# Performance work log

Hardware: AMD Instinct MI355X
Metric: run time of the kernel (lower is better)

The kernel has to match this reference:

```python
import jax
jax.config.update("jax_enable_x64", True)
import jax.numpy as jnp
import numpy as np

SAMPLE_RATE = 44100
HOP = 512
B, N_MELS, T = 8, 128, 2048
L = T * HOP  # 1,048,576 samples


def _lerp_up(x, out_len):
    # torch F.interpolate(mode='linear', align_corners=True): [B,C,Tin]->[B,C,out_len]
    t_in = x.shape[-1]
    pos = jnp.arange(out_len, dtype=jnp.float64) * ((t_in - 1) / (out_len - 1))
    i0 = jnp.floor(pos).astype(jnp.int32)
    i1 = jnp.minimum(i0 + 1, t_in - 1)
    w = (pos - i0).astype(x.dtype)
    return x[..., i0] * (1 - w) + x[..., i1] * w


def _conv1d(x, w, b, pad):
    y = jax.lax.conv_general_dilated(x, w, (1,), [(pad, pad)],
                                     dimension_numbers=("NCH", "OIH", "NCH"))
    return y + b[None, :, None]


def setup_inputs() -> dict:
    key = jax.random.key(0)
    ks = jax.random.split(key, 9)
    mel_frames = jax.random.normal(ks[0], (B, N_MELS, T), dtype=jnp.float32)
    # realistic f0: 80..380 Hz
    f0_frames = 80.0 + 300.0 * jax.random.uniform(ks[1], (B, T), dtype=jnp.float32)
    noise = jax.random.normal(ks[2], (B, L), dtype=jnp.float32)
    w1 = jax.random.normal(ks[3], (128, N_MELS, 7), dtype=jnp.float32) * 0.05
    b1 = jnp.zeros((128,), jnp.float32)
    w2 = jax.random.normal(ks[4], (128, 128, 3), dtype=jnp.float32) * 0.05
    b2 = jnp.zeros((128,), jnp.float32)
    w3 = jax.random.normal(ks[5], (2, 128, 3), dtype=jnp.float32) * 0.05
    b3 = jnp.zeros((2,), jnp.float32)
    return {"mel_frames": mel_frames, "f0_frames": f0_frames, "noise": noise,
            "w1": w1, "b1": b1, "w2": w2, "b2": b2, "w3": w3, "b3": b3}


def reference(mel_frames, f0_frames, noise, w1, b1, w2, b2, w3, b3):
    # --- comb source ---
    f0 = _lerp_up(f0_frames[:, None, :], L)  # [B,1,L]
    phase = jnp.cumsum(f0.astype(jnp.float64) / SAMPLE_RATE, axis=-1)
    phase = phase - jnp.round(phase)
    phase = phase.astype(f0.dtype)
    combtooth = jnp.sinc(SAMPLE_RATE * phase / (f0 + 1e-8))[:, 0, :]  # [B,L]
    # --- magnitude network ---
    h = jax.nn.leaky_relu(_conv1d(mel_frames, w1, b1, 3), 0.2)
    h = jax.nn.leaky_relu(_conv1d(h, w2, b2, 1), 0.2)
    mags = jnp.clip(_conv1d(h, w3, b3, 1), 0.0, 1.0)  # [B,2,T]
    mags = _lerp_up(mags, L)  # [B,2,L]
    noise_sig = jnp.clip(noise * mags[:, 0, :], -1.0, 1.0)
    comb_sig = jnp.clip(combtooth * mags[:, 1, :], -1.0, 1.0)
    signal = jnp.clip(noise_sig + comb_sig, -1.0, 1.0)
    return (signal[:, None, :], (comb_sig[:, None, :], noise_sig[:, None, :]))
```

## Files before the change

### kernel.cpp

```cpp
#include <hip/hip_runtime.h>
#include <math.h>

#define BATCH 8
#define NMEL 128
#define TT 2048
#define LL 1048576
#define NCHUNK 256
#define CHUNK 4096

static constexpr double RATIO  = 2047.0 / 1048575.0;
static constexpr float  RATIOF = (float)(2047.0 / 1048575.0);
static constexpr double INV_SR = 1.0 / 44100.0;

__global__ __launch_bounds__(256) void wtrans_kernel(
    const float* __restrict__ w1, const float* __restrict__ w2,
    float* __restrict__ w1t, float* __restrict__ w2t)
{
    int i = blockIdx.x * 256 + threadIdx.x;
    if (i < 896 * 128) {
        int m = i >> 7, co = i & 127;
        w1t[i] = w1[co * 896 + m];
    }
    if (i < 384 * 128) {
        int m = i >> 7, co = i & 127;
        w2t[i] = w2[co * 384 + m];
    }
}

#define CONV_FMA(acc, wq, xv, K) \
    _Pragma("unroll") \
    for (int k = 0; k < K; ++k) { \
        float wv0 = wq[k].x, wv1 = wq[k].y, wv2 = wq[k].z, wv3 = wq[k].w; \
        _Pragma("unroll") \
        for (int i = 0; i < 5; ++i) { \
            acc[0][i] = fmaf(wv0, xv[i + k], acc[0][i]); \
            acc[1][i] = fmaf(wv1, xv[i + k], acc[1][i]); \
            acc[2][i] = fmaf(wv2, xv[i + k], acc[2][i]); \
            acc[3][i] = fmaf(wv3, xv[i + k], acc[3][i]); } }

#define XSTR 48
#define HSTR 44
__global__ __launch_bounds__(256, 3) void conv_chunk_kernel(
    const float* __restrict__ mel,
    const float* __restrict__ w1t,
    const float* __restrict__ b1,
    const float* __restrict__ w2t,
    const float* __restrict__ b2,
    const float* __restrict__ w3,
    const float* __restrict__ b3,
    float* __restrict__ mags,
    const float* __restrict__ f0f,
    double* __restrict__ sums)
{
    __shared__ __align__(16) float smem[NMEL * XSTR + NMEL * HSTR];
    int tid = threadIdx.x;
    int lane = tid & 63, wid = tid >> 6;

    if (blockIdx.x >= 512) {
        int cb = blockIdx.x - 512;
        int b = cb >> 8;
        int c = cb & (NCHUNK - 1);
        const float* row = f0f + b * TT;
        int start = c * CHUNK + tid * 16;
        double pos0 = (double)start * RATIO;
        int i0s = (int)pos0;
        float wb = (float)(pos0 - (double)i0s);
        int ib = i0s + 1 > TT - 1 ? TT - 1 : i0s + 1;
        int ic = i0s + 2 > TT - 1 ? TT - 1 : i0s + 2;
        float f0a = row[i0s], f0b = row[ib], f0c = row[ic];
        double s = 0.0;
        #pragma unroll
        for (int i = 0; i < 16; ++i) {
            float wi = wb + (float)i * RATIOF;
            bool hi = wi >= 1.0f;
            float w = hi ? wi - 1.0f : wi;
            float xa = hi ? f0b : f0a, xb = hi ? f0c : f0b;
            float f0 = xa * (1.0f - w) + xb * w;
            s += (double)f0 * INV_SR;
        }
        #pragma unroll
        for (int off = 32; off > 0; off >>= 1) s += __shfl_down(s, (unsigned)off, 64);
        double* dred = (double*)smem;
        if (lane == 0) dred[wid] = s;
        __syncthreads();
        if (tid == 0) sums[cb] = dred[0] + dred[1] + dred[2] + dred[3];
        return;
    }

    float* Xs  = smem;
    float* H1  = smem + NMEL * XSTR;
    float* H2  = smem;
    float* red = smem + NMEL * XSTR;

    int b  = blockIdx.x >> 6;
    int t0 = (blockIdx.x & 63) * 32;
    const float* melb = mel + (size_t)b * NMEL * TT;

    #pragma unroll
    for (int it = 0; it < 6; ++it) {
        int idx = tid + it * 256;
        int ci = idx / 12, q = idx - ci * 12;
        int t = t0 - 8 + q * 4;
        float4 v = make_float4(0.f, 0.f, 0.f, 0.f);
        if (t >= 0 && t + 3 < TT) v = *(const float4*)(melb + ci * TT + t);
        *(float4*)(&Xs[ci * XSTR + q * 4]) = v;
    }
    if (tid < 128) { H1[tid * HSTR + 0] = 0.f; H1[tid * HSTR + 41] = 0.f; }
    __syncthreads();

    int cog = tid >> 3;
    int tg  = tid & 7;
    int xbase = 1 + tg * 5;

    {
        float acc[4][5];
        #pragma unroll
        for (int j = 0; j < 4; ++j) {
            float bj = b1[cog * 4 + j];
            #pragma unroll
            for (int i = 0; i < 5; ++i) acc[j][i] = bj;
        }
        const float* wb_ = w1t + cog * 4;
        float xvA[11], xvB[11];
        float4 wA[7], wB[7];
        #pragma unroll
        for (int i = 0; i < 11; ++i) xvA[i] = Xs[xbase + i];
        #pragma unroll
        for (int k = 0; k < 7; ++k) wA[k] = *(const float4*)(wb_ + (size_t)k * 128);
        for (int ci = 0; ci < NMEL; ci += 2) {
            int c1 = ci + 1;
            #pragma unroll
            for (int i = 0; i < 11; ++i) xvB[i] = Xs[c1 * XSTR + xbase + i];
            #pragma unroll
            for (int k = 0; k < 7; ++k) wB[k] = *(const float4*)(wb_ + (size_t)(c1 * 7 + k) * 128);
            CONV_FMA(acc, wA, xvA, 7)
            int c2 = ci + 2 < NMEL ? ci + 2 : NMEL - 1;
            #pragma unroll
            for (int i = 0; i < 11; ++i) xvA[i] = Xs[c2 * XSTR + xbase + i];
            #pragma unroll
            for (int k = 0; k < 7; ++k) wA[k] = *(const float4*)(wb_ + (size_t)(c2 * 7 + k) * 128);
            CONV_FMA(acc, wB, xvB, 7)
        }
        #pragma unroll
        for (int j = 0; j < 4; ++j)
            #pragma unroll
            for (int i = 0; i < 5; ++i) {
                int t = t0 - 4 + tg * 5 + i;
                float v = acc[j][i];
                v = v > 0.0f ? v : 0.2f * v;
                if (t < 0 || t >= TT) v = 0.0f;
                H1[(cog * 4 + j) * HSTR + 1 + tg * 5 + i] = v;
            }
    }
    __syncthreads();

    {
        float acc[4][5];
        #pragma unroll
        for (int j = 0; j < 4; ++j) {
            float bj = b2[cog * 4 + j];
            #pragma unroll
            for (int i = 0; i < 5; ++i) acc[j][i] = bj;
        }
        int hbase = tg * 5;
        const float* wb_ = w2t + cog * 4;
        float xvA[7], xvB[7];
        float4 wA[3], wB[3];
        #pragma unroll
        for (int i = 0; i < 7; ++i) xvA[i] = H1[hbase + i];
        #pragma unroll
        for (int k = 0; k < 3; ++k) wA[k] = *(const float4*)(wb_ + (size_t)k * 128);
        for (int ci = 0; ci < NMEL; ci += 2) {
            int c1 = ci + 1;
            #pragma unroll
            for (int i = 0; i < 7; ++i) xvB[i] = H1[c1 * HSTR + hbase + i];
            #pragma unroll
            for (int k = 0; k < 3; ++k) wB[k] = *(const float4*)(wb_ + (size_t)(c1 * 3 + k) * 128);
            CONV_FMA(acc, wA, xvA, 3)
            int c2 = ci + 2 < NMEL ? ci + 2 : NMEL - 1;
            #pragma unroll
            for (int i = 0; i < 7; ++i) xvA[i] = H1[c2 * HSTR + hbase + i];
            #pragma unroll
            for (int k = 0; k < 3; ++k) wA[k] = *(const float4*)(wb_ + (size_t)(c2 * 3 + k) * 128);
            CONV_FMA(acc, wB, xvB, 3)
        }
        #pragma unroll
        for (int j = 0; j < 4; ++j)
            #pragma unroll
            for (int i = 0; i < 5; ++i) {
                int t = t0 - 4 + tg * 5 + i;
                float v = acc[j][i];
                v = v > 0.0f ? v : 0.2f * v;
                if (t < 0 || t >= TT) v = 0.0f;
                H2[(cog * 4 + j) * HSTR + tg * 5 + i] = v;
            }
    }
    __syncthreads();

    {
        int o   = tid >> 7;
        int cig = (tid >> 5) & 3;
        int tt  = tid & 31;
        float a = 0.0f;
        for (int cl = 0; cl < 32; ++cl) {
            int ci = cig * 32 + cl;
            #pragma unroll
            for (int k = 0; k < 3; ++k)
                a = fmaf(w3[o * 384 + ci * 3 + k], H2[ci * HSTR + tt + 3 + k], a);
        }
        red[(o * 4 + cig) * 32 + tt] = a;
    }
    __syncthreads();
    if (tid < 64) {
        int o = tid >> 5, tt = tid & 31;
        float s = b3[o] + red[(o * 4 + 0) * 32 + tt] + red[(o * 4 + 1) * 32 + tt]
                        + red[(o * 4 + 2) * 32 + tt] + red[(o * 4 + 3) * 32 + tt];
        s = fminf(fmaxf(s, 0.0f), 1.0f);
        mags[((size_t)b * 2 + o) * TT + t0 + tt] = s;
    }
}

__device__ __forceinline__ int swz4(int g) { return g ^ ((g >> 3) & 7); }

__global__ __launch_bounds__(256, 4) void final_kernel(
    const float* __restrict__ f0f,
    const float* __restrict__ noise,
    const float* __restrict__ mags,
    const double* __restrict__ sums,
    float* __restrict__ out)
{
    int b = blockIdx.x >> 8;
    int c = blockIdx.x & (NCHUNK - 1);
    const float* row = f0f + b * TT;
    int tid = threadIdx.x;
    int lane = tid & 63, wid = tid >> 6;
    __shared__ float4 fracsV[CHUNK / 4];
    __shared__ double wsumP[4], wsumA[4];

    int chunkBase = c * CHUNK;
    int start = chunkBase + tid * 16;

    double part = (tid < c) ? sums[b * NCHUNK + tid] : 0.0;
    #pragma unroll
    for (int off = 32; off > 0; off >>= 1) part += __shfl_down(part, (unsigned)off, 64);
    if (lane == 0) wsumP[wid] = part;

    double pos0 = (double)start * RATIO;
    int i0s = (int)pos0;
    float wb = (float)(pos0 - (double)i0s);
    int ibk = i0s + 1 > TT - 1 ? TT - 1 : i0s + 1;
    int ick = i0s + 2 > TT - 1 ? TT - 1 : i0s + 2;
    float f0a = row[i0s], f0b = row[ibk], f0c = row[ick];
    float f0v[16];
    double s = 0.0;
    #pragma unroll
    for (int i = 0; i < 16; ++i) {
        float wi = wb + (float)i * RATIOF;
        bool hi = wi >= 1.0f;
        float w = hi ? wi - 1.0f : wi;
        float xa = hi ? f0b : f0a, xb = hi ? f0c : f0b;
        f0v[i] = xa * (1.0f - w) + xb * w;
        s += (double)f0v[i] * INV_SR;
    }
    double incl = s;
    #pragma unroll
    for (int off = 1; off < 64; off <<= 1) {
        double v = __shfl_up(incl, (unsigned)off, 64);
        if (lane >= off) incl += v;
    }
    if (lane == 63) wsumA[wid] = incl;
    __syncthreads();
    double run = wsumP[0] + wsumP[1] + wsumP[2] + wsumP[3] + (incl - s);
    for (int w = 0; w < wid; ++w) run += wsumA[w];

    float fb[4];
    #pragma unroll
    for (int i = 0; i < 16; ++i) {
        run += (double)f0v[i] * INV_SR;
        double fr = run - rint(run);
        fb[i & 3] = (float)fr;
        if ((i & 3) == 3)
            fracsV[swz4(tid * 4 + (i >> 2))] = make_float4(fb[0], fb[1], fb[2], fb[3]);
    }
    __syncthreads();

    const size_t BL = (size_t)BATCH * LL;
    const size_t outBase = (size_t)b * LL;
    const float* m0row = mags + (size_t)b * 2 * TT;
    const float* m1row = m0row + TT;

    #pragma unroll
    for (int g = 0; g < 4; ++g) {
        int G = g * 256 + tid;
        int n0 = chunkBase + G * 4;
        float4 fr4 = fracsV[swz4(G)];
        const float* frp = (const float*)&fr4;
        float4 nz4 = *(const float4*)(noise + outBase + n0);
        const float* nzp = (const float*)&nz4;

        double posg = (double)n0 * RATIO;
        int i0a = (int)posg;
        float wf = (float)(posg - (double)i0a);
        int ib = i0a + 1 > TT - 1 ? TT - 1 : i0a + 1;
        int ic = i0a + 2 > TT - 1 ? TT - 1 : i0a + 2;
        float g0a = row[i0a],   g0b = row[ib],   g0c = row[ic];
        float m0a = m0row[i0a], m0b = m0row[ib], m0c = m0row[ic];
        float m1a = m1row[i0a], m1b = m1row[ib], m1c = m1row[ic];

        float so[4], co_[4], no_[4];
        #pragma unroll
        for (int j = 0; j < 4; ++j) {
            float wj = wf + (float)j * RATIOF;
            bool hi = wj >= 1.0f;
            float w = hi ? wj - 1.0f : wj;
            float xa = hi ? g0b : g0a, xb = hi ? g0c : g0b;
            float f0 = xa * (1.0f - w) + xb * w;
            float ya = hi ? m0b : m0a, yb = hi ? m0c : m0b;
            float m0 = ya * (1.0f - w) + yb * w;
            float za = hi ? m1b : m1a, zb = hi ? m1c : m1b;
            float m1 = za * (1.0f - w) + zb * w;

            float ph = frp[j];
            float x  = 44100.0f * ph * __builtin_amdgcn_rcpf(f0 + 1e-8f);
            float px = 3.14159265358979323f * x;
            float rr = 0.5f * x;
            float rf = rr - rintf(rr);
            float sn;
            asm("v_sin_f32 %0, %1" : "=v"(sn) : "v"(rf));
            float comb = (x == 0.0f) ? 1.0f : sn * __builtin_amdgcn_rcpf(px);

            float ns = fminf(fmaxf(nzp[j] * m0, -1.0f), 1.0f);
            float cs = fminf(fmaxf(comb * m1, -1.0f), 1.0f);
            so[j] = fminf(fmaxf(ns + cs, -1.0f), 1.0f);
            co_[j] = cs; no_[j] = ns;
        }
        *(float4*)(out + outBase + n0)          = make_float4(so[0], so[1], so[2], so[3]);
        *(float4*)(out + BL + outBase + n0)     = make_float4(co_[0], co_[1], co_[2], co_[3]);
        *(float4*)(out + 2 * BL + outBase + n0) = make_float4(no_[0], no_[1], no_[2], no_[3]);
    }
}

extern "C" void kernel_launch(void* const* d_in, const int* in_sizes, int n_in,
                              void* d_out, int out_size, void* d_ws, size_t ws_size,
                              hipStream_t stream) {
    const float* mel   = (const float*)d_in[0];
    const float* f0f   = (const float*)d_in[1];
    const float* noise = (const float*)d_in[2];
    const float* w1    = (const float*)d_in[3];
    const float* b1    = (const float*)d_in[4];
    const float* w2    = (const float*)d_in[5];
    const float* b2    = (const float*)d_in[6];
    const float* w3    = (const float*)d_in[7];
    const float* b3    = (const float*)d_in[8];
    float* out = (float*)d_out;

    float* w1t  = (float*)d_ws;
    float* w2t  = w1t + 896 * 128;
    float* mags = w2t + 384 * 128;
    double* sums = (double*)(mags + BATCH * 2 * TT);

    wtrans_kernel<<<(896 * 128 + 255) / 256, 256, 0, stream>>>(w1, w2, w1t, w2t);
    conv_chunk_kernel<<<512 + BATCH * NCHUNK, 256, 0, stream>>>(
        mel, w1t, b1, w2t, b2, w3, b3, mags, f0f, sums);
    final_kernel<<<BATCH * NCHUNK, 256, 0, stream>>>(f0f, noise, mags, sums, out);
}
```

Before: 261.6 us.

## Split final kernel into phase and output passes; simplify conv loops

The final kernel is split in two. One kernel computes the wrapped phase fractions and writes them to a global workspace buffer of B*L floats. A second kernel reads them back together with noise and mags to produce the outputs. This removes the shared-memory staging and a block barrier, at the cost of an extra 32 MB global write and read plus one more launch. The conv loops also drop manual double-buffering in favour of a simple loop with unroll 2, leaving scheduling to the compiler.

Result: no change. 265.8 us (+1.6%).

```diff
diff --git a/kernel.cpp b/kernel.cpp
--- a/kernel.cpp
+++ b/kernel.cpp
@@ -26,17 +26,6 @@
         w2t[i] = w2[co * 384 + m];
     }
 }
-
-#define CONV_FMA(acc, wq, xv, K) \
-    _Pragma("unroll") \
-    for (int k = 0; k < K; ++k) { \
-        float wv0 = wq[k].x, wv1 = wq[k].y, wv2 = wq[k].z, wv3 = wq[k].w; \
-        _Pragma("unroll") \
-        for (int i = 0; i < 5; ++i) { \
-            acc[0][i] = fmaf(wv0, xv[i + k], acc[0][i]); \
-            acc[1][i] = fmaf(wv1, xv[i + k], acc[1][i]); \
-            acc[2][i] = fmaf(wv2, xv[i + k], acc[2][i]); \
-            acc[3][i] = fmaf(wv3, xv[i + k], acc[3][i]); } }
 
 #define XSTR 48
 #define HSTR 44
@@ -120,26 +109,22 @@
             #pragma unroll
             for (int i = 0; i < 5; ++i) acc[j][i] = bj;
         }
-        const float* wb_ = w1t + cog * 4;
-        float xvA[11], xvB[11];
-        float4 wA[7], wB[7];
-        #pragma unroll
-        for (int i = 0; i < 11; ++i) xvA[i] = Xs[xbase + i];
-        #pragma unroll
-        for (int k = 0; k < 7; ++k) wA[k] = *(const float4*)(wb_ + (size_t)k * 128);
-        for (int ci = 0; ci < NMEL; ci += 2) {
-            int c1 = ci + 1;
-            #pragma unroll
-            for (int i = 0; i < 11; ++i) xvB[i] = Xs[c1 * XSTR + xbase + i];
-            #pragma unroll
-            for (int k = 0; k < 7; ++k) wB[k] = *(const float4*)(wb_ + (size_t)(c1 * 7 + k) * 128);
-            CONV_FMA(acc, wA, xvA, 7)
-            int c2 = ci + 2 < NMEL ? ci + 2 : NMEL - 1;
-            #pragma unroll
-            for (int i = 0; i < 11; ++i) xvA[i] = Xs[c2 * XSTR + xbase + i];
-            #pragma unroll
-            for (int k = 0; k < 7; ++k) wA[k] = *(const float4*)(wb_ + (size_t)(c2 * 7 + k) * 128);
-            CONV_FMA(acc, wB, xvB, 7)
+        #pragma unroll 2
+        for (int ci = 0; ci < NMEL; ++ci) {
+            float xv[11];
+            #pragma unroll
+            for (int i = 0; i < 11; ++i) xv[i] = Xs[ci * XSTR + xbase + i];
+            const float* wr = w1t + (size_t)(ci * 7) * 128 + cog * 4;
+            #pragma unroll
+            for (int k = 0; k < 7; ++k) {
+                float4 w4 = *(const float4*)(wr + k * 128);
+                float wv[4] = {w4.x, w4.y, w4.z, w4.w};
+                #pragma unroll
+                for (int j = 0; j < 4; ++j)
+                    #pragma unroll
+                    for (int i = 0; i < 5; ++i)
+                        acc[j][i] = fmaf(wv[j], xv[i + k], acc[j][i]);
+            }
         }
         #pragma unroll
         for (int j = 0; j < 4; ++j)
@@ -163,26 +148,22 @@
             for (int i = 0; i < 5; ++i) acc[j][i] = bj;
         }
         int hbase = tg * 5;
-        const float* wb_ = w2t + cog * 4;
-        float xvA[7], xvB[7];
-        float4 wA[3], wB[3];
-        #pragma unroll
-        for (int i = 0; i < 7; ++i) xvA[i] = H1[hbase + i];
-        #pragma unroll
-        for (int k = 0; k < 3; ++k) wA[k] = *(const float4*)(wb_ + (size_t)k * 128);
-        for (int ci = 0; ci < NMEL; ci += 2) {
-            int c1 = ci + 1;
-            #pragma unroll
-            for (int i = 0; i < 7; ++i) xvB[i] = H1[c1 * HSTR + hbase + i];
-            #pragma unroll
-            for (int k = 0; k < 3; ++k) wB[k] = *(const float4*)(wb_ + (size_t)(c1 * 3 + k) * 128);
-            CONV_FMA(acc, wA, xvA, 3)
-            int c2 = ci + 2 < NMEL ? ci + 2 : NMEL - 1;
-            #pragma unroll
-            for (int i = 0; i < 7; ++i) xvA[i] = H1[c2 * HSTR + hbase + i];
-            #pragma unroll
-            for (int k = 0; k < 3; ++k) wA[k] = *(const float4*)(wb_ + (size_t)(c2 * 3 + k) * 128);
-            CONV_FMA(acc, wB, xvB, 3)
+        #pragma unroll 2
+        for (int ci = 0; ci < NMEL; ++ci) {
+            float xv[7];
+            #pragma unroll
+            for (int i = 0; i < 7; ++i) xv[i] = H1[ci * HSTR + hbase + i];
+            const float* wr = w2t + (size_t)(ci * 3) * 128 + cog * 4;
+            #pragma unroll
+            for (int k = 0; k < 3; ++k) {
+                float4 w4 = *(const float4*)(wr + k * 128);
+                float wv[4] = {w4.x, w4.y, w4.z, w4.w};
+                #pragma unroll
+                for (int j = 0; j < 4; ++j)
+                    #pragma unroll
+                    for (int i = 0; i < 5; ++i)
+                        acc[j][i] = fmaf(wv[j], xv[i + k], acc[j][i]);
+            }
         }
         #pragma unroll
         for (int j = 0; j < 4; ++j)
@@ -220,21 +201,16 @@
     }
 }
 
-__device__ __forceinline__ int swz4(int g) { return g ^ ((g >> 3) & 7); }
-
-__global__ __launch_bounds__(256, 4) void final_kernel(
+__global__ __launch_bounds__(256, 4) void finalA_kernel(
     const float* __restrict__ f0f,
-    const float* __restrict__ noise,
-    const float* __restrict__ mags,
     const double* __restrict__ sums,
-    float* __restrict__ out)
+    float* __restrict__ fracs)
 {
     int b = blockIdx.x >> 8;
     int c = blockIdx.x & (NCHUNK - 1);
     const float* row = f0f + b * TT;
     int tid = threadIdx.x;
     int lane = tid & 63, wid = tid >> 6;
-    __shared__ float4 fracsV[CHUNK / 4];
     __shared__ double wsumP[4], wsumA[4];
 
     int chunkBase = c * CHUNK;
@@ -273,16 +249,30 @@
     double run = wsumP[0] + wsumP[1] + wsumP[2] + wsumP[3] + (incl - s);
     for (int w = 0; w < wid; ++w) run += wsumA[w];
 
-    float fb[4];
+    float* fg = fracs + (size_t)b * LL + start;
+    float fb4[4];
     #pragma unroll
     for (int i = 0; i < 16; ++i) {
         run += (double)f0v[i] * INV_SR;
         double fr = run - rint(run);
-        fb[i & 3] = (float)fr;
+        fb4[i & 3] = (float)fr;
         if ((i & 3) == 3)
-            fracsV[swz4(tid * 4 + (i >> 2))] = make_float4(fb[0], fb[1], fb[2], fb[3]);
-    }
-    __syncthreads();
+            *(float4*)(fg + (i & ~3)) = make_float4(fb4[0], fb4[1], fb4[2], fb4[3]);
+    }
+}
+
+__global__ __launch_bounds__(256, 4) void finalB_kernel(
+    const float* __restrict__ f0f,
+    const float* __restrict__ noise,
+    const float* __restrict__ mags,
+    const float* __restrict__ fracs,
+    float* __restrict__ out)
+{
+    int b = blockIdx.x >> 8;
+    int c = blockIdx.x & (NCHUNK - 1);
+    const float* row = f0f + b * TT;
+    int tid = threadIdx.x;
+    int chunkBase = c * CHUNK;
 
     const size_t BL = (size_t)BATCH * LL;
     const size_t outBase = (size_t)b * LL;
@@ -293,7 +283,7 @@
     for (int g = 0; g < 4; ++g) {
         int G = g * 256 + tid;
         int n0 = chunkBase + G * 4;
-        float4 fr4 = fracsV[swz4(G)];
+        float4 fr4 = *(const float4*)(fracs + outBase + n0);
         const float* frp = (const float*)&fr4;
         float4 nz4 = *(const float4*)(noise + outBase + n0);
         const float* nzp = (const float*)&nz4;
@@ -358,9 +348,11 @@
     float* w2t  = w1t + 896 * 128;
     float* mags = w2t + 384 * 128;
     double* sums = (double*)(mags + BATCH * 2 * TT);
+    float* fracs = (float*)(sums + BATCH * NCHUNK);
 
     wtrans_kernel<<<(896 * 128 + 255) / 256, 256, 0, stream>>>(w1, w2, w1t, w2t);
     conv_chunk_kernel<<<512 + BATCH * NCHUNK, 256, 0, stream>>>(
         mel, w1t, b1, w2t, b2, w3, b3, mags, f0f, sums);
-    final_kernel<<<BATCH * NCHUNK, 256, 0, stream>>>(f0f, noise, mags, sums, out);
-}
+    finalA_kernel<<<BATCH * NCHUNK, 256, 0, stream>>>(f0f, sums, fracs);
+    finalB_kernel<<<BATCH * NCHUNK, 256, 0, stream>>>(f0f, noise, mags, fracs, out);
+}
```
